# Performance work log

Measured on AMD Instinct MI355X. Metric: run time of the kernel, lower is better.

## Reference

```python
import jax, jax.numpy as jnp
import numpy as np

D_MODEL = 1024
N_HEAD = 16
HEAD_DIM = D_MODEL // N_HEAD
ROPE_BASE = 10000.0


def _weight_quant(w):
    # BitNet b1.58 ternary weight quant with per-tensor absmean scale (STE).
    scale = jnp.clip(jnp.mean(jnp.abs(w)), 1e-5, None)
    wq = jnp.clip(jnp.round(w / scale), -1.0, 1.0) * scale
    return w + jax.lax.stop_gradient(wq - w)


def _act_quant(x):
    # Per-token int8 absmax activation quant (STE).
    scale = 127.0 / jnp.clip(jnp.max(jnp.abs(x), axis=-1, keepdims=True), 1e-5, None)
    xq = jnp.clip(jnp.round(x * scale), -128.0, 127.0) / scale
    return x + jax.lax.stop_gradient(xq - x)


def _bitlinear(x, w):
    # y = act_quant(x) @ weight_quant(w).T   (torch Linear convention, no bias)
    return _act_quant(x) @ _weight_quant(w).T


def _rope(x, pos):
    # x: [B, H, T, D]; half-split rotation.
    d = x.shape[-1]
    inv_freq = 1.0 / (ROPE_BASE ** (jnp.arange(0, d, 2, dtype=jnp.float32) / d))
    ang = pos[:, None].astype(jnp.float32) * inv_freq[None, :]  # [T, D/2]
    cos, sin = jnp.cos(ang), jnp.sin(ang)
    x1, x2 = x[..., : d // 2], x[..., d // 2 :]
    return jnp.concatenate([x1 * cos - x2 * sin, x1 * sin + x2 * cos], axis=-1)


def setup_inputs() -> dict:
    key = jax.random.key(0)
    k0, k1, k2, k3, k4 = jax.random.split(key, 5)
    B, T = 2, 2048
    s = 1.0 / np.sqrt(D_MODEL)
    return {
        "x": jax.random.normal(k0, (B, T, D_MODEL), dtype=jnp.float32),
        "Wq": jax.random.normal(k1, (D_MODEL, D_MODEL), dtype=jnp.float32) * s,
        "Wk": jax.random.normal(k2, (D_MODEL, D_MODEL), dtype=jnp.float32) * s,
        "Wv": jax.random.normal(k3, (D_MODEL, D_MODEL), dtype=jnp.float32) * s,
        "Wo": jax.random.normal(k4, (D_MODEL, D_MODEL), dtype=jnp.float32) * s,
    }


def reference(x, Wq, Wk, Wv, Wo):
    B, T, C = x.shape
    pos = jnp.arange(T)
    def heads(y):
        return y.reshape(B, T, N_HEAD, HEAD_DIM).transpose(0, 2, 1, 3)  # [B,H,T,D]
    q = _rope(heads(_bitlinear(x, Wq)), pos)
    k = _rope(heads(_bitlinear(x, Wk)), pos)
    v = heads(_bitlinear(x, Wv))
    scores = jnp.einsum("bhqd,bhkd->bhqk", q, k) / jnp.sqrt(jnp.float32(HEAD_DIM))
    causal = jnp.tril(jnp.ones((T, T), dtype=bool))
    scores = jnp.where(causal[None, None], scores, jnp.finfo(scores.dtype).min)
    att = jax.nn.softmax(scores, axis=-1)
    y = jnp.einsum("bhqk,bhkd->bhqd", att, v)  # [B,H,T,D]
    y = y.transpose(0, 2, 1, 3).reshape(B, T, C)
    return _bitlinear(y, Wo)
```

## Files before the change

### kernel.cpp

```cpp
#include <hip/hip_runtime.h>
#include <hip/hip_bf16.h>
#include <math.h>

typedef __bf16 bf16_t;
typedef __attribute__((ext_vector_type(8))) __bf16 bf16x8;
typedef __attribute__((ext_vector_type(4))) __bf16 bf16x4;
typedef __attribute__((ext_vector_type(4))) float f32x4;

typedef __attribute__((address_space(3))) void lds_void_t;
typedef const __attribute__((address_space(1))) void glb_void_t;
#define GLOAD_LDS(g, l) __builtin_amdgcn_global_load_lds((glb_void_t*)(g), (lds_void_t*)(l), 16, 0, 0)

#define MFMA16(a,b,c) __builtin_amdgcn_mfma_f32_16x16x32_bf16(a,b,c,0,0,0)

#if __has_builtin(__builtin_amdgcn_exp2f)
#define EXP2F(x) __builtin_amdgcn_exp2f(x)
#else
#define EXP2F(x) exp2f(x)
#endif

static constexpr int TSEQ = 2048;
static constexpr int CDIM = 1024;
#define NEG_BIG (-1.0e30f)
#define Q_PRESCALE 0.18033688011112042f
#define ROPE_C 0.41524101190971284f

__global__ __launch_bounds__(256) void wreduce(const float* __restrict__ W0, const float* __restrict__ W1,
                                               const float* __restrict__ W2, const float* __restrict__ W3,
                                               double* __restrict__ partial) {
  int w = blockIdx.x >> 6, b = blockIdx.x & 63;
  const float* W = (w==0)?W0:(w==1)?W1:(w==2)?W2:W3;
  const float* base = W + (size_t)b * 16384;
  double s = 0.0;
  for (int i = threadIdx.x * 4; i < 16384; i += 1024) {
    float4 v = *(const float4*)(base + i);
    s += (double)fabsf(v.x) + (double)fabsf(v.y) + (double)fabsf(v.z) + (double)fabsf(v.w);
  }
  #pragma unroll
  for (int off = 1; off < 64; off <<= 1) s += __shfl_xor(s, off);
  __shared__ double red[4];
  if ((threadIdx.x & 63) == 0) red[threadIdx.x >> 6] = s;
  __syncthreads();
  if (threadIdx.x == 0) partial[blockIdx.x] = red[0] + red[1] + red[2] + red[3];
}

__global__ __launch_bounds__(256) void prep(const float* __restrict__ W0, const float* __restrict__ W1,
                                            const float* __restrict__ W2, const float* __restrict__ W3,
                                            const double* __restrict__ partial, float* __restrict__ wscale,
                                            bf16_t* __restrict__ wq_all,
                                            const float* __restrict__ xg, bf16_t* __restrict__ xqg,
                                            float* __restrict__ rowfac, float2* __restrict__ ropetab) {
  int bid = blockIdx.x;
  if (bid < 4096) {
    int w = bid >> 10;
    double ssum = 0.0;
    for (int i = 0; i < 64; ++i) ssum += partial[w * 64 + i];
    float s = fmaxf((float)(ssum * (1.0 / 1048576.0)), 1e-5f);
    if ((bid & 1023) == 0 && threadIdx.x == 0) wscale[w] = s;
    const float* W = (w==0)?W0:(w==1)?W1:(w==2)?W2:W3;
    int off = ((bid & 1023) * 256 + threadIdx.x) * 4;
    float4 v = *(const float4*)(W + off);
    bf16x4 q;
    q[0] = (bf16_t)fminf(fmaxf(rintf(v.x / s), -1.f), 1.f);
    q[1] = (bf16_t)fminf(fmaxf(rintf(v.y / s), -1.f), 1.f);
    q[2] = (bf16_t)fminf(fmaxf(rintf(v.z / s), -1.f), 1.f);
    q[3] = (bf16_t)fminf(fmaxf(rintf(v.w / s), -1.f), 1.f);
    *(bf16x4*)(wq_all + (size_t)w * 1048576 + off) = q;
  } else if (bid < 8192) {
    int r = bid - 4096;
    float4 v = *(const float4*)(xg + (size_t)r * 1024 + threadIdx.x * 4);
    float mx = fmaxf(fmaxf(fabsf(v.x), fabsf(v.y)), fmaxf(fabsf(v.z), fabsf(v.w)));
    #pragma unroll
    for (int off = 1; off < 64; off <<= 1) mx = fmaxf(mx, __shfl_xor(mx, off));
    __shared__ float red[4];
    if ((threadIdx.x & 63) == 0) red[threadIdx.x >> 6] = mx;
    __syncthreads();
    mx = fmaxf(fmaxf(red[0], red[1]), fmaxf(red[2], red[3]));
    mx = fmaxf(mx, 1e-5f);
    float scale = 127.0f / mx;
    if (threadIdx.x == 0) rowfac[r] = mx * (1.0f / 127.0f);
    bf16x4 q;
    q[0] = (bf16_t)fminf(fmaxf(rintf(v.x * scale), -128.f), 127.f);
    q[1] = (bf16_t)fminf(fmaxf(rintf(v.y * scale), -128.f), 127.f);
    q[2] = (bf16_t)fminf(fmaxf(rintf(v.z * scale), -128.f), 127.f);
    q[3] = (bf16_t)fminf(fmaxf(rintf(v.w * scale), -128.f), 127.f);
    *(bf16x4*)(xqg + (size_t)r * 1024 + threadIdx.x * 4) = q;
  } else {
    int t = (bid - 8192) * 8 + (threadIdx.x >> 5);
    int ii = threadIdx.x & 31;
    float ang = (float)t * exp2f(-(float)ii * ROPE_C);
    float sn, cs;
    sincosf(ang, &sn, &cs);
    ropetab[t * 32 + ii] = make_float2(cs, sn);
  }
}

__global__ __launch_bounds__(256) void actquant(const float* __restrict__ xg, bf16_t* __restrict__ xqg,
                                                float* __restrict__ rowfac) {
  int r = blockIdx.x;
  float4 v = *(const float4*)(xg + (size_t)r * 1024 + threadIdx.x * 4);
  float mx = fmaxf(fmaxf(fabsf(v.x), fabsf(v.y)), fmaxf(fabsf(v.z), fabsf(v.w)));
  #pragma unroll
  for (int off = 1; off < 64; off <<= 1) mx = fmaxf(mx, __shfl_xor(mx, off));
  __shared__ float red[4];
  if ((threadIdx.x & 63) == 0) red[threadIdx.x >> 6] = mx;
  __syncthreads();
  mx = fmaxf(fmaxf(red[0], red[1]), fmaxf(red[2], red[3]));
  mx = fmaxf(mx, 1e-5f);
  float scale = 127.0f / mx;
  if (threadIdx.x == 0) rowfac[r] = mx * (1.0f / 127.0f);
  bf16x4 q;
  q[0] = (bf16_t)fminf(fmaxf(rintf(v.x * scale), -128.f), 127.f);
  q[1] = (bf16_t)fminf(fmaxf(rintf(v.y * scale), -128.f), 127.f);
  q[2] = (bf16_t)fminf(fmaxf(rintf(v.z * scale), -128.f), 127.f);
  q[3] = (bf16_t)fminf(fmaxf(rintf(v.w * scale), -128.f), 127.f);
  *(bf16x4*)(xqg + (size_t)r * 1024 + threadIdx.x * 4) = q;
}

__global__ __launch_bounds__(256) void gemm_qkv(const bf16_t* __restrict__ xq, const bf16_t* __restrict__ wq_all,
                                                const float* __restrict__ wscale, const float* __restrict__ rowfac,
                                                const float2* __restrict__ ropetab,
                                                bf16_t* __restrict__ qb, bf16_t* __restrict__ kb,
                                                bf16_t* __restrict__ vtb) {
  const int z = blockIdx.z;
  const bf16_t* Bw = wq_all + (size_t)z * 1048576;
  const int m0 = blockIdx.x * 128, n0 = blockIdx.y * 128;
  const int tid = threadIdx.x;
  const int wave = tid >> 6, lane = tid & 63, quad = lane >> 4, l16 = lane & 15;
  const int wm = wave >> 1, wn = wave & 1;
  __shared__ __align__(16) bf16_t As[128 * 32];
  __shared__ __align__(16) bf16_t Bs[128 * 32];
  f32x4 zero = {0.f, 0.f, 0.f, 0.f};
  f32x4 acc[4][4];
  #pragma unroll
  for (int i = 0; i < 4; ++i)
    #pragma unroll
    for (int j = 0; j < 4; ++j) acc[i][j] = zero;

  const int row_s = tid >> 2;
  const int cg8 = (((tid & 3) - (row_s >> 1)) & 3) * 8;
  const int sw8 = ((quad + (l16 >> 1)) & 3) * 8;

  for (int kt = 0; kt < 32; ++kt) {
    __syncthreads();
    #pragma unroll
    for (int v2 = 0; v2 < 2; ++v2) {
      int v = tid + v2 * 256;
      int row = row_s + v2 * 64;
      GLOAD_LDS(&xq[(size_t)(m0 + row) * 1024 + kt * 32 + cg8], &As[v * 8]);
      GLOAD_LDS(&Bw[(size_t)(n0 + row) * 1024 + kt * 32 + cg8], &Bs[v * 8]);
    }
    __syncthreads();
    bf16x8 af[4], bfr[4];
    #pragma unroll
    for (int i = 0; i < 4; ++i) af[i] = *(const bf16x8*)&As[(wm * 64 + i * 16 + l16) * 32 + sw8];
    #pragma unroll
    for (int j = 0; j < 4; ++j) bfr[j] = *(const bf16x8*)&Bs[(wn * 64 + j * 16 + l16) * 32 + sw8];
    if (z == 2) {
      #pragma unroll
      for (int i = 0; i < 4; ++i)
        #pragma unroll
        for (int j = 0; j < 4; ++j) acc[i][j] = MFMA16(bfr[i], af[j], acc[i][j]);
    } else {
      #pragma unroll
      for (int i = 0; i < 4; ++i)
        #pragma unroll
        for (int j = 0; j < 4; ++j) acc[i][j] = MFMA16(af[i], bfr[j], acc[i][j]);
    }
  }
  float ws = wscale[z] * (z == 0 ? Q_PRESCALE : 1.0f);
  if (z <= 1) {
    bf16_t* dst = (z == 0) ? qb : kb;
    const int h = (n0 >> 6) + wn;
    #pragma unroll
    for (int i = 0; i < 4; ++i) {
      #pragma unroll
      for (int r = 0; r < 4; ++r) {
        int m = m0 + wm * 64 + i * 16 + quad * 4 + r;
        float rf = rowfac[m] * ws;
        int b = m >> 11, t = m & 2047;
        bf16_t* drow = dst + (((size_t)b * 16 + h) * 2048 + t) * 64;
        #pragma unroll
        for (int j = 0; j < 2; ++j) {
          int dd1 = j * 16 + l16;
          float2 cs2 = ropetab[t * 32 + dd1];
          float v1 = acc[i][j][r] * rf;
          float v2 = acc[i][j + 2][r] * rf;
          drow[dd1]      = (bf16_t)(v1 * cs2.x - v2 * cs2.y);
          drow[dd1 + 32] = (bf16_t)(v1 * cs2.y + v2 * cs2.x);
        }
      }
    }
  } else {
    const int b = m0 >> 11;
    const int tbase = (m0 & 2047) + wm * 64;
    float rfj[4];
    #pragma unroll
    for (int j = 0; j < 4; ++j) rfj[j] = rowfac[m0 + wm * 64 + j * 16 + l16] * ws;
    #pragma unroll
    for (int i = 0; i < 4; ++i) {
      #pragma unroll
      for (int r = 0; r < 4; ++r) {
        int nrow = n0 + wn * 64 + i * 16 + quad * 4 + r;
        int h = nrow >> 6, dd = nrow & 63;
        bf16_t* vrow = vtb + (((size_t)b * 16 + h) * 64 + dd) * 2048 + tbase;
        #pragma unroll
        for (int j = 0; j < 4; ++j) vrow[j * 16 + l16] = (bf16_t)(acc[i][j][r] * rfj[j]);
      }
    }
  }
}

__global__ __launch_bounds__(256) void gemm_out(const bf16_t* __restrict__ yq, const bf16_t* __restrict__ wo,
                                                const float* __restrict__ wscale, const float* __restrict__ rowfac,
                                                float* __restrict__ out) {
  const int m0 = blockIdx.x * 128, n0 = blockIdx.y * 128;
  const int tid = threadIdx.x;
  const int wave = tid >> 6, lane = tid & 63, quad = lane >> 4, l16 = lane & 15;
  const int wm = wave >> 1, wn = wave & 1;
  __shared__ __align__(16) bf16_t As[128 * 32];
  __shared__ __align__(16) bf16_t Bs[128 * 32];
  f32x4 zero = {0.f, 0.f, 0.f, 0.f};
  f32x4 acc[4][4];
  #pragma unroll
  for (int i = 0; i < 4; ++i)
    #pragma unroll
    for (int j = 0; j < 4; ++j) acc[i][j] = zero;

  const int row_s = tid >> 2;
  const int cg8 = (((tid & 3) - (row_s >> 1)) & 3) * 8;
  const int sw8 = ((quad + (l16 >> 1)) & 3) * 8;

  for (int kt = 0; kt < 32; ++kt) {
    __syncthreads();
    #pragma unroll
    for (int v2 = 0; v2 < 2; ++v2) {
      int v = tid + v2 * 256;
      int row = row_s + v2 * 64;
      GLOAD_LDS(&yq[(size_t)(m0 + row) * 1024 + kt * 32 + cg8], &As[v * 8]);
      GLOAD_LDS(&wo[(size_t)(n0 + row) * 1024 + kt * 32 + cg8], &Bs[v * 8]);
    }
    __syncthreads();
    bf16x8 af[4], bfr[4];
    #pragma unroll
    for (int i = 0; i < 4; ++i) af[i] = *(const bf16x8*)&As[(wm * 64 + i * 16 + l16) * 32 + sw8];
    #pragma unroll
    for (int j = 0; j < 4; ++j) bfr[j] = *(const bf16x8*)&Bs[(wn * 64 + j * 16 + l16) * 32 + sw8];
    #pragma unroll
    for (int i = 0; i < 4; ++i)
      #pragma unroll
      for (int j = 0; j < 4; ++j) acc[i][j] = MFMA16(af[i], bfr[j], acc[i][j]);
  }
  float ws = wscale[3];
  #pragma unroll
  for (int i = 0; i < 4; ++i) {
    #pragma unroll
    for (int r = 0; r < 4; ++r) {
      int m = m0 + wm * 64 + i * 16 + quad * 4 + r;
      float rf = rowfac[m] * ws;
      #pragma unroll
      for (int j = 0; j < 4; ++j) {
        int n = n0 + wn * 64 + j * 16 + l16;
        out[(size_t)m * 1024 + n] = acc[i][j][r] * rf;
      }
    }
  }
}

__global__ __launch_bounds__(512) void flash_attn(const bf16_t* __restrict__ qg, const bf16_t* __restrict__ kg,
                                                  const bf16_t* __restrict__ vtg, float* __restrict__ yf) {
  const int p = blockIdx.x;
  const int bh = blockIdx.y;
  const int tid = threadIdx.x;
  const int wave = tid >> 6, lane = tid & 63;
  const int quad = lane >> 4, l16 = lane & 15;

  __shared__ __align__(16) bf16_t Kb[2][64 * 64];
  __shared__ __align__(16) bf16_t Vb[2][64 * 64];
  __shared__ __align__(16) bf16_t Pl[8][16 * 72];

  const int b = bh >> 4, h = bh & 15;
  bf16_t* Pw = &Pl[wave][0];

  const int r0 = tid >> 3, cblk = tid & 7;
  const int ldsOff0 = r0 * 64 + ((cblk ^ (r0 & 7)) * 8);
  const size_t bhbase = (size_t)bh * 131072;
  const bf16_t* kbase0 = kg + bhbase + r0 * 64 + cblk * 8;
  const bf16_t* vbase0 = vtg + bhbase + r0 * 2048 + cblk * 8;

  int kf_off[4][2];
  #pragma unroll
  for (int n = 0; n < 4; ++n)
    #pragma unroll
    for (int c = 0; c < 2; ++c)
      kf_off[n][c] = (n * 16 + l16) * 64 + (((c * 4 + quad) ^ (l16 & 7)) * 8);

  bf16x8 ones;
  #pragma unroll
  for (int j = 0; j < 8; ++j) ones[j] = (bf16_t)1.0f;
  f32x4 zero = {0.f, 0.f, 0.f, 0.f};

  bf16x8 kpre = *(const bf16x8*)(kbase0);
  bf16x8 vpre = *(const bf16x8*)(vbase0);

  int cum = 0;
  #pragma unroll 1
  for (int tsel = 0; tsel < 2; ++tsel) {
    const int qt = tsel ? (15 - p) : p;
    const int kcmax = 2 * qt + 1;
    const int qbw = qt * 128 + wave * 16;

    const bf16_t* qrowp = qg + ((size_t)bh * TSEQ + qbw + l16) * 64;
    bf16x8 aq0 = *(const bf16x8*)(qrowp + quad * 8);
    bf16x8 aq1 = *(const bf16x8*)(qrowp + 32 + quad * 8);

    f32x4 o[4], o5;
    #pragma unroll
    for (int i = 0; i < 4; ++i) o[i] = zero;
    o5 = zero;

    #pragma unroll 1
    for (int kc = 0; kc <= kcmax; ++kc, ++cum) {
      const int buf = cum & 1;
      bf16_t* Kt = &Kb[buf][0];
      bf16_t* Vt = &Vb[buf][0];
      *(bf16x8*)&Kt[ldsOff0] = kpre;
      *(bf16x8*)&Vt[ldsOff0] = vpre;
      __syncthreads();
      int nkc = (kc < kcmax) ? (kc + 1) : ((tsel == 0) ? 0 : -1);
      if (nkc >= 0) {
        kpre = *(const bf16x8*)(kbase0 + nkc * 4096);
        vpre = *(const bf16x8*)(vbase0 + nkc * 64);
      }

      f32x4 s[4];
      #pragma unroll
      for (int n = 0; n < 4; ++n) {
        bf16x8 bk0 = *(const bf16x8*)&Kt[kf_off[n][0]];
        bf16x8 bk1 = *(const bf16x8*)&Kt[kf_off[n][1]];
        s[n] = MFMA16(aq1, bk1, MFMA16(aq0, bk0, zero));
      }
      if (kc * 64 + 63 > qbw) {
        #pragma unroll
        for (int n = 0; n < 4; ++n)
          #pragma unroll
          for (int r = 0; r < 4; ++r) {
            int kpos = kc * 64 + n * 16 + l16;
            int qpos = qbw + quad * 4 + r;
            if (kpos > qpos) s[n][r] = NEG_BIG;
          }
      }
      #pragma unroll
      for (int n = 0; n < 4; ++n)
        #pragma unroll
        for (int r = 0; r < 4; ++r)
          Pw[(quad * 4 + r) * 72 + n * 16 + l16] = (bf16_t)EXP2F(s[n][r]);

      bf16x8 ap0 = *(const bf16x8*)&Pw[l16 * 72 + quad * 8];
      bf16x8 ap1 = *(const bf16x8*)&Pw[l16 * 72 + 32 + quad * 8];
      #pragma unroll
      for (int nh = 0; nh < 4; ++nh) {
        bf16x8 bv0 = *(const bf16x8*)&Vt[kf_off[nh][0]];
        bf16x8 bv1 = *(const bf16x8*)&Vt[kf_off[nh][1]];
        o[nh] = MFMA16(ap1, bv1, MFMA16(ap0, bv0, o[nh]));
      }
      o5 = MFMA16(ap1, ones, MFMA16(ap0, ones, o5));
    }

    #pragma unroll
    for (int r = 0; r < 4; ++r) {
      float invl = 1.0f / o5[r];
      int t = qbw + quad * 4 + r;
      float* yrow = yf + ((size_t)b * TSEQ + t) * CDIM + h * 64;
      #pragma unroll
      for (int nh = 0; nh < 4; ++nh) yrow[nh * 16 + l16] = o[nh][r] * invl;
    }
  }
}

extern "C" void kernel_launch(void* const* d_in, const int* in_sizes, int n_in,
                              void* d_out, int out_size, void* d_ws, size_t ws_size,
                              hipStream_t stream) {
  const float* x  = (const float*)d_in[0];
  const float* Wq = (const float*)d_in[1];
  const float* Wk = (const float*)d_in[2];
  const float* Wv = (const float*)d_in[3];
  const float* Wo = (const float*)d_in[4];
  float* out = (float*)d_out;

  char* ws = (char*)d_ws;
  double* wpartial = (double*)(ws);
  float* wscale   = (float*)(ws + 4096);
  float* rowfacx  = (float*)(ws + 8192);
  float* rowfacy  = (float*)(ws + 8192 + 16384);
  bf16_t* wq_all  = (bf16_t*)(ws + 65536);
  bf16_t* xq      = wq_all + 4194304;
  bf16_t* qb      = xq + 4194304;
  bf16_t* kb      = qb + 4194304;
  bf16_t* vtb     = kb + 4194304;
  float*  yf      = (float*)(vtb + 4194304);
  float2* ropetab = (float2*)(yf + 4194304);
  bf16_t* yq      = xq;

  wreduce<<<256, 256, 0, stream>>>(Wq, Wk, Wv, Wo, wpartial);
  prep<<<8448, 256, 0, stream>>>(Wq, Wk, Wv, Wo, wpartial, wscale, wq_all, x, xq, rowfacx, ropetab);
  gemm_qkv<<<dim3(32, 8, 3), 256, 0, stream>>>(xq, wq_all, wscale, rowfacx, ropetab, qb, kb, vtb);
  flash_attn<<<dim3(8, 32), 512, 0, stream>>>(qb, kb, vtb, yf);
  actquant<<<4096, 256, 0, stream>>>(yf, yq, rowfacy);
  gemm_out<<<dim3(32, 8), 256, 0, stream>>>(yq, wq_all + 3 * 1048576, wscale, rowfacy, out);
}
```

Before: 206.2 us.

## Switch BitNet GEMMs to int8 MFMA with int8 quantized operands

Quantized weights and activations are stored as int8 instead of bf16, and the QKV and output GEMMs use the i32 16x16x64 int8 MFMA with K-tiles of 64 bytes per row. This halves the operand bytes moved and doubles the K covered per instruction; the results stay exact because the values are small integers accumulated in int32. The flash-attention block index is also remapped so that consecutive blocks spread across heads and query tiles, which changes scheduling and cache behavior.

```diff
diff --git a/kernel.cpp b/kernel.cpp
--- a/kernel.cpp
+++ b/kernel.cpp
@@ -3,15 +3,18 @@
 #include <math.h>
 
 typedef __bf16 bf16_t;
+typedef signed char i8_t;
 typedef __attribute__((ext_vector_type(8))) __bf16 bf16x8;
 typedef __attribute__((ext_vector_type(4))) __bf16 bf16x4;
 typedef __attribute__((ext_vector_type(4))) float f32x4;
+typedef __attribute__((ext_vector_type(4))) int i32x4;
 
 typedef __attribute__((address_space(3))) void lds_void_t;
 typedef const __attribute__((address_space(1))) void glb_void_t;
 #define GLOAD_LDS(g, l) __builtin_amdgcn_global_load_lds((glb_void_t*)(g), (lds_void_t*)(l), 16, 0, 0)
 
 #define MFMA16(a,b,c) __builtin_amdgcn_mfma_f32_16x16x32_bf16(a,b,c,0,0,0)
+#define MFMAI8(a,b,c) __builtin_amdgcn_mfma_i32_16x16x64_i8(a,b,c,0,0,0)
 
 #if __has_builtin(__builtin_amdgcn_exp2f)
 #define EXP2F(x) __builtin_amdgcn_exp2f(x)
@@ -47,8 +50,8 @@
 __global__ __launch_bounds__(256) void prep(const float* __restrict__ W0, const float* __restrict__ W1,
                                             const float* __restrict__ W2, const float* __restrict__ W3,
                                             const double* __restrict__ partial, float* __restrict__ wscale,
-                                            bf16_t* __restrict__ wq_all,
-                                            const float* __restrict__ xg, bf16_t* __restrict__ xqg,
+                                            i8_t* __restrict__ wq_all,
+                                            const float* __restrict__ xg, i8_t* __restrict__ xqg,
                                             float* __restrict__ rowfac, float2* __restrict__ ropetab) {
   int bid = blockIdx.x;
   if (bid < 4096) {
@@ -60,12 +63,12 @@
     const float* W = (w==0)?W0:(w==1)?W1:(w==2)?W2:W3;
     int off = ((bid & 1023) * 256 + threadIdx.x) * 4;
     float4 v = *(const float4*)(W + off);
-    bf16x4 q;
-    q[0] = (bf16_t)fminf(fmaxf(rintf(v.x / s), -1.f), 1.f);
-    q[1] = (bf16_t)fminf(fmaxf(rintf(v.y / s), -1.f), 1.f);
-    q[2] = (bf16_t)fminf(fmaxf(rintf(v.z / s), -1.f), 1.f);
-    q[3] = (bf16_t)fminf(fmaxf(rintf(v.w / s), -1.f), 1.f);
-    *(bf16x4*)(wq_all + (size_t)w * 1048576 + off) = q;
+    char4 q;
+    q.x = (i8_t)(int)fminf(fmaxf(rintf(v.x / s), -1.f), 1.f);
+    q.y = (i8_t)(int)fminf(fmaxf(rintf(v.y / s), -1.f), 1.f);
+    q.z = (i8_t)(int)fminf(fmaxf(rintf(v.z / s), -1.f), 1.f);
+    q.w = (i8_t)(int)fminf(fmaxf(rintf(v.w / s), -1.f), 1.f);
+    *(char4*)(wq_all + (size_t)w * 1048576 + off) = q;
   } else if (bid < 8192) {
     int r = bid - 4096;
     float4 v = *(const float4*)(xg + (size_t)r * 1024 + threadIdx.x * 4);
@@ -79,12 +82,12 @@
     mx = fmaxf(mx, 1e-5f);
     float scale = 127.0f / mx;
     if (threadIdx.x == 0) rowfac[r] = mx * (1.0f / 127.0f);
-    bf16x4 q;
-    q[0] = (bf16_t)fminf(fmaxf(rintf(v.x * scale), -128.f), 127.f);
-    q[1] = (bf16_t)fminf(fmaxf(rintf(v.y * scale), -128.f), 127.f);
-    q[2] = (bf16_t)fminf(fmaxf(rintf(v.z * scale), -128.f), 127.f);
-    q[3] = (bf16_t)fminf(fmaxf(rintf(v.w * scale), -128.f), 127.f);
-    *(bf16x4*)(xqg + (size_t)r * 1024 + threadIdx.x * 4) = q;
+    char4 q;
+    q.x = (i8_t)(int)fminf(fmaxf(rintf(v.x * scale), -128.f), 127.f);
+    q.y = (i8_t)(int)fminf(fmaxf(rintf(v.y * scale), -128.f), 127.f);
+    q.z = (i8_t)(int)fminf(fmaxf(rintf(v.z * scale), -128.f), 127.f);
+    q.w = (i8_t)(int)fminf(fmaxf(rintf(v.w * scale), -128.f), 127.f);
+    *(char4*)(xqg + (size_t)r * 1024 + threadIdx.x * 4) = q;
   } else {
     int t = (bid - 8192) * 8 + (threadIdx.x >> 5);
     int ii = threadIdx.x & 31;
@@ -95,7 +98,7 @@
   }
 }
 
-__global__ __launch_bounds__(256) void actquant(const float* __restrict__ xg, bf16_t* __restrict__ xqg,
+__global__ __launch_bounds__(256) void actquant(const float* __restrict__ xg, i8_t* __restrict__ xqg,
                                                 float* __restrict__ rowfac) {
   int r = blockIdx.x;
   float4 v = *(const float4*)(xg + (size_t)r * 1024 + threadIdx.x * 4);
@@ -109,63 +112,63 @@
   mx = fmaxf(mx, 1e-5f);
   float scale = 127.0f / mx;
   if (threadIdx.x == 0) rowfac[r] = mx * (1.0f / 127.0f);
-  bf16x4 q;
-  q[0] = (bf16_t)fminf(fmaxf(rintf(v.x * scale), -128.f), 127.f);
-  q[1] = (bf16_t)fminf(fmaxf(rintf(v.y * scale), -128.f), 127.f);
-  q[2] = (bf16_t)fminf(fmaxf(rintf(v.z * scale), -128.f), 127.f);
-  q[3] = (bf16_t)fminf(fmaxf(rintf(v.w * scale), -128.f), 127.f);
-  *(bf16x4*)(xqg + (size_t)r * 1024 + threadIdx.x * 4) = q;
-}
-
-__global__ __launch_bounds__(256) void gemm_qkv(const bf16_t* __restrict__ xq, const bf16_t* __restrict__ wq_all,
+  char4 q;
+  q.x = (i8_t)(int)fminf(fmaxf(rintf(v.x * scale), -128.f), 127.f);
+  q.y = (i8_t)(int)fminf(fmaxf(rintf(v.y * scale), -128.f), 127.f);
+  q.z = (i8_t)(int)fminf(fmaxf(rintf(v.z * scale), -128.f), 127.f);
+  q.w = (i8_t)(int)fminf(fmaxf(rintf(v.w * scale), -128.f), 127.f);
+  *(char4*)(xqg + (size_t)r * 1024 + threadIdx.x * 4) = q;
+}
+
+__global__ __launch_bounds__(256) void gemm_qkv(const i8_t* __restrict__ xq, const i8_t* __restrict__ wq_all,
                                                 const float* __restrict__ wscale, const float* __restrict__ rowfac,
                                                 const float2* __restrict__ ropetab,
                                                 bf16_t* __restrict__ qb, bf16_t* __restrict__ kb,
                                                 bf16_t* __restrict__ vtb) {
   const int z = blockIdx.z;
-  const bf16_t* Bw = wq_all + (size_t)z * 1048576;
+  const i8_t* Bw = wq_all + (size_t)z * 1048576;
   const int m0 = blockIdx.x * 128, n0 = blockIdx.y * 128;
   const int tid = threadIdx.x;
   const int wave = tid >> 6, lane = tid & 63, quad = lane >> 4, l16 = lane & 15;
   const int wm = wave >> 1, wn = wave & 1;
-  __shared__ __align__(16) bf16_t As[128 * 32];
-  __shared__ __align__(16) bf16_t Bs[128 * 32];
-  f32x4 zero = {0.f, 0.f, 0.f, 0.f};
-  f32x4 acc[4][4];
+  __shared__ __align__(16) i8_t As[128 * 64];
+  __shared__ __align__(16) i8_t Bs[128 * 64];
+  i32x4 zero = {0, 0, 0, 0};
+  i32x4 acc[4][4];
   #pragma unroll
   for (int i = 0; i < 4; ++i)
     #pragma unroll
     for (int j = 0; j < 4; ++j) acc[i][j] = zero;
 
   const int row_s = tid >> 2;
-  const int cg8 = (((tid & 3) - (row_s >> 1)) & 3) * 8;
-  const int sw8 = ((quad + (l16 >> 1)) & 3) * 8;
-
-  for (int kt = 0; kt < 32; ++kt) {
+  const int cg16 = (((tid & 3) - (row_s >> 1)) & 3) * 16;
+  const int sw16 = ((quad + (l16 >> 1)) & 3) * 16;
+
+  for (int kt = 0; kt < 16; ++kt) {
     __syncthreads();
     #pragma unroll
     for (int v2 = 0; v2 < 2; ++v2) {
       int v = tid + v2 * 256;
       int row = row_s + v2 * 64;
-      GLOAD_LDS(&xq[(size_t)(m0 + row) * 1024 + kt * 32 + cg8], &As[v * 8]);
-      GLOAD_LDS(&Bw[(size_t)(n0 + row) * 1024 + kt * 32 + cg8], &Bs[v * 8]);
+      GLOAD_LDS(&xq[(size_t)(m0 + row) * 1024 + kt * 64 + cg16], &As[v * 16]);
+      GLOAD_LDS(&Bw[(size_t)(n0 + row) * 1024 + kt * 64 + cg16], &Bs[v * 16]);
     }
     __syncthreads();
-    bf16x8 af[4], bfr[4];
-    #pragma unroll
-    for (int i = 0; i < 4; ++i) af[i] = *(const bf16x8*)&As[(wm * 64 + i * 16 + l16) * 32 + sw8];
-    #pragma unroll
-    for (int j = 0; j < 4; ++j) bfr[j] = *(const bf16x8*)&Bs[(wn * 64 + j * 16 + l16) * 32 + sw8];
+    i32x4 af[4], bfr[4];
+    #pragma unroll
+    for (int i = 0; i < 4; ++i) af[i] = *(const i32x4*)&As[(wm * 64 + i * 16 + l16) * 64 + sw16];
+    #pragma unroll
+    for (int j = 0; j < 4; ++j) bfr[j] = *(const i32x4*)&Bs[(wn * 64 + j * 16 + l16) * 64 + sw16];
     if (z == 2) {
       #pragma unroll
       for (int i = 0; i < 4; ++i)
         #pragma unroll
-        for (int j = 0; j < 4; ++j) acc[i][j] = MFMA16(bfr[i], af[j], acc[i][j]);
+        for (int j = 0; j < 4; ++j) acc[i][j] = MFMAI8(bfr[i], af[j], acc[i][j]);
     } else {
       #pragma unroll
       for (int i = 0; i < 4; ++i)
         #pragma unroll
-        for (int j = 0; j < 4; ++j) acc[i][j] = MFMA16(af[i], bfr[j], acc[i][j]);
+        for (int j = 0; j < 4; ++j) acc[i][j] = MFMAI8(af[i], bfr[j], acc[i][j]);
     }
   }
   float ws = wscale[z] * (z == 0 ? Q_PRESCALE : 1.0f);
@@ -184,8 +187,8 @@
         for (int j = 0; j < 2; ++j) {
           int dd1 = j * 16 + l16;
           float2 cs2 = ropetab[t * 32 + dd1];
-          float v1 = acc[i][j][r] * rf;
-          float v2 = acc[i][j + 2][r] * rf;
+          float v1 = (float)acc[i][j][r] * rf;
+          float v2 = (float)acc[i][j + 2][r] * rf;
           drow[dd1]      = (bf16_t)(v1 * cs2.x - v2 * cs2.y);
           drow[dd1 + 32] = (bf16_t)(v1 * cs2.y + v2 * cs2.x);
         }
@@ -205,51 +208,51 @@
         int h = nrow >> 6, dd = nrow & 63;
         bf16_t* vrow = vtb + (((size_t)b * 16 + h) * 64 + dd) * 2048 + tbase;
         #pragma unroll
-        for (int j = 0; j < 4; ++j) vrow[j * 16 + l16] = (bf16_t)(acc[i][j][r] * rfj[j]);
-      }
-    }
-  }
-}
-
-__global__ __launch_bounds__(256) void gemm_out(const bf16_t* __restrict__ yq, const bf16_t* __restrict__ wo,
+        for (int j = 0; j < 4; ++j) vrow[j * 16 + l16] = (bf16_t)((float)acc[i][j][r] * rfj[j]);
+      }
+    }
+  }
+}
+
+__global__ __launch_bounds__(256) void gemm_out(const i8_t* __restrict__ yq, const i8_t* __restrict__ wo,
                                                 const float* __restrict__ wscale, const float* __restrict__ rowfac,
                                                 float* __restrict__ out) {
   const int m0 = blockIdx.x * 128, n0 = blockIdx.y * 128;
   const int tid = threadIdx.x;
   const int wave = tid >> 6, lane = tid & 63, quad = lane >> 4, l16 = lane & 15;
   const int wm = wave >> 1, wn = wave & 1;
-  __shared__ __align__(16) bf16_t As[128 * 32];
-  __shared__ __align__(16) bf16_t Bs[128 * 32];
-  f32x4 zero = {0.f, 0.f, 0.f, 0.f};
-  f32x4 acc[4][4];
+  __shared__ __align__(16) i8_t As[128 * 64];
+  __shared__ __align__(16) i8_t Bs[128 * 64];
+  i32x4 zero = {0, 0, 0, 0};
+  i32x4 acc[4][4];
   #pragma unroll
   for (int i = 0; i < 4; ++i)
     #pragma unroll
     for (int j = 0; j < 4; ++j) acc[i][j] = zero;
 
   const int row_s = tid >> 2;
-  const int cg8 = (((tid & 3) - (row_s >> 1)) & 3) * 8;
-  const int sw8 = ((quad + (l16 >> 1)) & 3) * 8;
-
-  for (int kt = 0; kt < 32; ++kt) {
+  const int cg16 = (((tid & 3) - (row_s >> 1)) & 3) * 16;
+  const int sw16 = ((quad + (l16 >> 1)) & 3) * 16;
+
+  for (int kt = 0; kt < 16; ++kt) {
     __syncthreads();
     #pragma unroll
     for (int v2 = 0; v2 < 2; ++v2) {
       int v = tid + v2 * 256;
       int row = row_s + v2 * 64;
-      GLOAD_LDS(&yq[(size_t)(m0 + row) * 1024 + kt * 32 + cg8], &As[v * 8]);
-      GLOAD_LDS(&wo[(size_t)(n0 + row) * 1024 + kt * 32 + cg8], &Bs[v * 8]);
+      GLOAD_LDS(&yq[(size_t)(m0 + row) * 1024 + kt * 64 + cg16], &As[v * 16]);
+      GLOAD_LDS(&wo[(size_t)(n0 + row) * 1024 + kt * 64 + cg16], &Bs[v * 16]);
     }
     __syncthreads();
-    bf16x8 af[4], bfr[4];
-    #pragma unroll
-    for (int i = 0; i < 4; ++i) af[i] = *(const bf16x8*)&As[(wm * 64 + i * 16 + l16) * 32 + sw8];
-    #pragma unroll
-    for (int j = 0; j < 4; ++j) bfr[j] = *(const bf16x8*)&Bs[(wn * 64 + j * 16 + l16) * 32 + sw8];
+    i32x4 af[4], bfr[4];
+    #pragma unroll
+    for (int i = 0; i < 4; ++i) af[i] = *(const i32x4*)&As[(wm * 64 + i * 16 + l16) * 64 + sw16];
+    #pragma unroll
+    for (int j = 0; j < 4; ++j) bfr[j] = *(const i32x4*)&Bs[(wn * 64 + j * 16 + l16) * 64 + sw16];
     #pragma unroll
     for (int i = 0; i < 4; ++i)
       #pragma unroll
-      for (int j = 0; j < 4; ++j) acc[i][j] = MFMA16(af[i], bfr[j], acc[i][j]);
+      for (int j = 0; j < 4; ++j) acc[i][j] = MFMAI8(af[i], bfr[j], acc[i][j]);
   }
   float ws = wscale[3];
   #pragma unroll
@@ -261,7 +264,7 @@
       #pragma unroll
       for (int j = 0; j < 4; ++j) {
         int n = n0 + wn * 64 + j * 16 + l16;
-        out[(size_t)m * 1024 + n] = acc[i][j][r] * rf;
+        out[(size_t)m * 1024 + n] = (float)acc[i][j][r] * rf;
       }
     }
   }
@@ -269,8 +272,9 @@
 
 __global__ __launch_bounds__(512) void flash_attn(const bf16_t* __restrict__ qg, const bf16_t* __restrict__ kg,
                                                   const bf16_t* __restrict__ vtg, float* __restrict__ yf) {
-  const int p = blockIdx.x;
-  const int bh = blockIdx.y;
+  const int lid = (int)blockIdx.y * 8 + (int)blockIdx.x;
+  const int p  = (lid >> 3) & 7;
+  const int bh = (lid & 7) * 4 + (lid >> 6);
   const int tid = threadIdx.x;
   const int wave = tid >> 6, lane = tid & 63;
   const int quad = lane >> 4, l16 = lane & 15;
@@ -393,14 +397,14 @@
   float* wscale   = (float*)(ws + 4096);
   float* rowfacx  = (float*)(ws + 8192);
   float* rowfacy  = (float*)(ws + 8192 + 16384);
-  bf16_t* wq_all  = (bf16_t*)(ws + 65536);
-  bf16_t* xq      = wq_all + 4194304;
-  bf16_t* qb      = xq + 4194304;
+  i8_t* wq_all    = (i8_t*)(ws + 65536);
+  i8_t* xq        = wq_all + 4194304;
+  bf16_t* qb      = (bf16_t*)(xq + 4194304);
   bf16_t* kb      = qb + 4194304;
   bf16_t* vtb     = kb + 4194304;
   float*  yf      = (float*)(vtb + 4194304);
   float2* ropetab = (float2*)(yf + 4194304);
-  bf16_t* yq      = xq;
+  i8_t* yq        = xq;
 
   wreduce<<<256, 256, 0, stream>>>(Wq, Wk, Wv, Wo, wpartial);
   prep<<<8448, 256, 0, stream>>>(Wq, Wk, Wv, Wo, wpartial, wscale, wq_all, x, xq, rowfacx, ropetab);
```

New measurement: 174.0 us. -15.6%, faster.
